# Performance work log

Measured on AMD Instinct MI355X. Metric: run time of the kernel, lower is better.

The kernel has to match this reference:

```python
import jax, jax.numpy as jnp
import numpy as np

B, D = 16384, 512
NUM_CLASSES, K = 90, 32


def _l2norm(v, axis=-1):
    return v / jnp.sqrt(jnp.sum(v * v, axis=axis, keepdims=True) + 1e-12)


def setup_inputs() -> dict:
    key = jax.random.key(0)
    k1, k2, k3 = jax.random.split(key, 3)
    x = jax.random.normal(k1, (B, D), dtype=jnp.float32)
    labels = jax.random.randint(k2, (B,), 0, NUM_CLASSES, dtype=jnp.int64)
    centers = jax.random.normal(k3, (NUM_CLASSES, K, D), dtype=jnp.float32)
    return {"x": x, "labels": labels, "centers": centers}


def reference(x, labels, centers):
    # l2Norm applied to centers at init and to x in forward
    xn = _l2norm(x, axis=1)                       # [B, D]
    cn = _l2norm(centers, axis=-1)                # [C, K, D]
    c = cn[labels]                                # gather: [B, K, D]
    # dst_k = 1 - <x_b, center_{label_b, k}>
    dst = 1.0 - jnp.einsum("bd,bkd->bk", xn, c)   # [B, K]
    score = jax.nn.softmax(2.0 - dst, axis=1)     # softmax over K sub-centers
    per_sample = jnp.sum(score * dst, axis=1)     # [B]
    return jnp.mean(per_sample)                   # scalar loss
```

## Files before the change

### kernel.cpp

```cpp
#include <hip/hip_runtime.h>
#include <hip/hip_bf16.h>

#define BB 16384
#define DD 512
#define NCLS 90
#define KC 32
#define BUCKET 512
#define PRB 180

typedef __attribute__((ext_vector_type(8))) short short8;
typedef __attribute__((ext_vector_type(4))) float fx4;

static __device__ __forceinline__ short f2bf(float f) {
    unsigned u = __float_as_uint(f);
    unsigned r = (u + 0x7fffu + ((u >> 16) & 1u)) >> 16;
    return (short)r;
}
static __device__ __forceinline__ short8 pack8(float4 a, float4 b) {
    union { __hip_bfloat162 h[4]; short8 s; } u;
    u.h[0] = __float22bfloat162_rn(make_float2(a.x, a.y));
    u.h[1] = __float22bfloat162_rn(make_float2(a.z, a.w));
    u.h[2] = __float22bfloat162_rn(make_float2(b.x, b.y));
    u.h[3] = __float22bfloat162_rn(make_float2(b.z, b.w));
    return u.s;
}
static __device__ __forceinline__ void gload_lds16(const void* g, void* l) {
    __builtin_amdgcn_global_load_lds(
        (const __attribute__((address_space(1))) void*)g,
        (__attribute__((address_space(3))) void*)l, 16, 0, 0);
}

__global__ __launch_bounds__(1024)
void k_prep(const float* __restrict__ centers, const int* __restrict__ labels,
            short* __restrict__ cni, int* __restrict__ idx, int* __restrict__ cnt) {
    __shared__ int lab[BB];
    __shared__ int wcnt[16];

    int t = threadIdx.x, w = t >> 6, lane = t & 63;

    if ((int)blockIdx.x < PRB) {
        int row = blockIdx.x * 16 + w;
        const float4* p = (const float4*)(centers + (size_t)row * DD);
        float4 a = p[lane * 2];
        float4 b = p[lane * 2 + 1];
        float s = a.x * a.x + a.y * a.y + a.z * a.z + a.w * a.w
                + b.x * b.x + b.y * b.y + b.z * b.z + b.w * b.w;
#pragma unroll
        for (int m = 1; m < 64; m <<= 1) s += __shfl_xor(s, m, 64);
        float sc = rsqrtf(s + 1e-12f);
        short8 v;
        v[0] = f2bf(a.x * sc); v[1] = f2bf(a.y * sc);
        v[2] = f2bf(a.z * sc); v[3] = f2bf(a.w * sc);
        v[4] = f2bf(b.x * sc); v[5] = f2bf(b.y * sc);
        v[6] = f2bf(b.z * sc); v[7] = f2bf(b.w * sc);
        *(short8*)(cni + (size_t)row * DD + lane * 8) = v;
    } else {
        int c = blockIdx.x - PRB;
        for (int j = t; j < BB / 4; j += 1024)
            ((int4*)lab)[j] = ((const int4*)labels)[j];
        __syncthreads();

        int seg4 = w * (BB / 4 / 16);
        int cw = 0;
#pragma unroll
        for (int jj = 0; jj < 4; jj++) {
            int4 v = ((int4*)lab)[seg4 + jj * 64 + lane];
            cw += (v.x == c) + (v.y == c) + (v.z == c) + (v.w == c);
        }
#pragma unroll
        for (int m = 1; m < 64; m <<= 1) cw += __shfl_xor(cw, m, 64);
        if (lane == 0) wcnt[w] = cw;
        __syncthreads();
        int pos = c * BUCKET;
        for (int ww = 0; ww < w; ww++) pos += wcnt[ww];
#pragma unroll
        for (int jj = 0; jj < 4; jj++) {
            int4 v = ((int4*)lab)[seg4 + jj * 64 + lane];
            int gbase = (seg4 + jj * 64 + lane) * 4;
            { bool m = (v.x == c); unsigned long long k = __ballot(m);
              if (m) idx[pos + __popcll(k & ((1ull << lane) - 1ull))] = gbase;     pos += __popcll(k); }
            { bool m = (v.y == c); unsigned long long k = __ballot(m);
              if (m) idx[pos + __popcll(k & ((1ull << lane) - 1ull))] = gbase + 1; pos += __popcll(k); }
            { bool m = (v.z == c); unsigned long long k = __ballot(m);
              if (m) idx[pos + __popcll(k & ((1ull << lane) - 1ull))] = gbase + 2; pos += __popcll(k); }
            { bool m = (v.w == c); unsigned long long k = __ballot(m);
              if (m) idx[pos + __popcll(k & ((1ull << lane) - 1ull))] = gbase + 3; pos += __popcll(k); }
        }
        if (t == 0) {
            int s = 0;
#pragma unroll
            for (int i = 0; i < 16; i++) s += wcnt[i];
            cnt[c] = s;
        }
    }
}

__launch_bounds__(256, 2)
__global__ void k_main(const float* __restrict__ x,
                       const short* __restrict__ cni,
                       const int* __restrict__ cnt,
                       const int* __restrict__ idx,
                       float* __restrict__ partials) {
    __shared__ __align__(16) short c_lds[KC * DD];
    __shared__ __align__(16) short x_lds[32 * DD];
    __shared__ float S_lds[32][33];
    __shared__ float xinv[32];
    __shared__ float red[256];

    int c = blockIdx.x >> 3;
    int p = blockIdx.x & 7;
    int n = cnt[c];
    int nch = (n + 31) >> 5;
    int t = threadIdx.x, w = t >> 6, lane = t & 63;
    float loss_acc = 0.f;

    if (p < nch) {
        const short* cbase = cni + (size_t)c * KC * DD;
#pragma unroll
        for (int it = 0; it < 8; it++) {
            int q = t + 256 * it;
            int drow = q >> 6, cc = q & 63;
            gload_lds16(cbase + drow * DD + (cc ^ (drow & 7)) * 8, &c_lds[q * 8]);
        }

        int base = c * BUCKET;
        int mrow = ((w & 1) << 4) + (lane & 15);
        int nrow = ((w >> 1) << 4) + (lane & 15);
        int row8 = t >> 3, l8 = t & 7;

        for (int ch = p; ch < nch; ch += 8) {
            int off = ch << 5;
            int rem = n - off;

            {
                int r = (row8 < rem) ? row8 : (rem - 1);
                int g = idx[base + off + r];
                const float4* src = (const float4*)(x + (size_t)g * DD);
                float4 va[8], vb[8];
#pragma unroll
                for (int jj = 0; jj < 8; jj++) {
                    va[jj] = src[2 * l8 + 16 * jj];
                    vb[jj] = src[2 * l8 + 16 * jj + 1];
                }
                float nrm = 0.f;
#pragma unroll
                for (int jj = 0; jj < 8; jj++) {
                    int cc = l8 + 8 * jj;
                    float4 a = va[jj], b = vb[jj];
                    nrm += a.x * a.x + a.y * a.y + a.z * a.z + a.w * a.w
                         + b.x * b.x + b.y * b.y + b.z * b.z + b.w * b.w;
                    *(short8*)&x_lds[row8 * DD + ((cc ^ (row8 & 7)) << 3)] = pack8(a, b);
                }
#pragma unroll
                for (int m = 1; m < 8; m <<= 1) nrm += __shfl_xor(nrm, m, 64);
                if (l8 == 0) xinv[row8] = rsqrtf(nrm + 1e-12f);
            }
            __syncthreads();

            fx4 acc = {0.f, 0.f, 0.f, 0.f};
#pragma unroll
            for (int ks = 0; ks < 16; ks++) {
                int c16a = ks * 4 + (lane >> 4);
                short8 av = *(const short8*)&x_lds[mrow * DD + ((c16a ^ (mrow & 7)) << 3)];
                short8 bv = *(const short8*)&c_lds[nrow * DD + ((c16a ^ (nrow & 7)) << 3)];
                acc = __builtin_amdgcn_mfma_f32_16x16x32_bf16(av, bv, acc, 0, 0, 0);
            }
#pragma unroll
            for (int j = 0; j < 4; j++) {
                int r = ((w & 1) << 4) + ((lane >> 4) << 2) + j;
                int col = ((w >> 1) << 4) + (lane & 15);
                S_lds[r][col] = acc[j];
            }
            __syncthreads();

            {
                float xv = xinv[row8];
                int q4 = l8 << 2;
                float s0 = S_lds[row8][q4 + 0] * xv;
                float s1 = S_lds[row8][q4 + 1] * xv;
                float s2 = S_lds[row8][q4 + 2] * xv;
                float s3 = S_lds[row8][q4 + 3] * xv;
                float mx = fmaxf(fmaxf(s0, s1), fmaxf(s2, s3));
#pragma unroll
                for (int m = 1; m < 8; m <<= 1) mx = fmaxf(mx, __shfl_xor(mx, m, 64));
                float e0 = expf(s0 - mx), e1 = expf(s1 - mx);
                float e2 = expf(s2 - mx), e3 = expf(s3 - mx);
                float Z = e0 + e1 + e2 + e3;
                float num = e0 * (1.f - s0) + e1 * (1.f - s1)
                          + e2 * (1.f - s2) + e3 * (1.f - s3);
#pragma unroll
                for (int m = 1; m < 8; m <<= 1) {
                    Z += __shfl_xor(Z, m, 64);
                    num += __shfl_xor(num, m, 64);
                }
                if (l8 == 0 && row8 < rem) loss_acc += num / Z;
            }
            __syncthreads();
        }
    }

    red[t] = loss_acc;
    __syncthreads();
    for (int h = 128; h > 0; h >>= 1) {
        if (t < h) red[t] += red[t + h];
        __syncthreads();
    }
    if (t == 0) partials[blockIdx.x] = red[0];
}

__global__ void k_final(const float* __restrict__ partials, float* __restrict__ out) {
    __shared__ float red[256];
    int t = threadIdx.x;
    float s = 0.f;
    for (int i = t; i < NCLS * 8; i += 256) s += partials[i];
    red[t] = s;
    __syncthreads();
    for (int h = 128; h > 0; h >>= 1) {
        if (t < h) red[t] += red[t + h];
        __syncthreads();
    }
    if (t == 0) out[0] = red[0] * (1.0f / (float)BB);
}

extern "C" void kernel_launch(void* const* d_in, const int* in_sizes, int n_in,
                              void* d_out, int out_size, void* d_ws, size_t ws_size,
                              hipStream_t stream) {
    const float* x       = (const float*)d_in[0];
    const int*   labels  = (const int*)d_in[1];
    const float* centers = (const float*)d_in[2];
    float* out = (float*)d_out;

    char* ws = (char*)d_ws;
    short* cni      = (short*)(ws + 0);
    int*   idx      = (int*)(ws + 3145728);
    int*   cnt      = (int*)(ws + 3407872);
    float* partials = (float*)(ws + 3473408);

    k_prep<<<PRB + NCLS, 1024, 0, stream>>>(centers, labels, cni, idx, cnt);
    k_main<<<NCLS * 8, 256, 0, stream>>>(x, cni, cnt, idx, partials);
    k_final<<<1, 256, 0, stream>>>(partials, out);
}
```

Measured before the change: 27.86 us.

## Scatter x into class-sorted bf16 buffer in separate streaming kernel

Replaces the gather of fp32 x rows inside the main kernel with a new streaming kernel. It reads x in row order, normalises each row, converts it to bf16 and scatters it into a per-class bucketed, swizzled layout together with the inverse norms. The main kernel then fills LDS with contiguous async global-to-LDS loads instead of indexed fp32 loads plus conversion. This costs one extra kernel launch and an extra bf16 write and read of x (about 16 MB through global memory), but makes the main kernel's loads coalesced and halves their size.

```diff
diff --git a/kernel.cpp b/kernel.cpp
--- a/kernel.cpp
+++ b/kernel.cpp
@@ -32,7 +32,7 @@
 
 __global__ __launch_bounds__(1024)
 void k_prep(const float* __restrict__ centers, const int* __restrict__ labels,
-            short* __restrict__ cni, int* __restrict__ idx, int* __restrict__ cnt) {
+            short* __restrict__ cni, int* __restrict__ dest, int* __restrict__ cnt) {
     __shared__ int lab[BB];
     __shared__ int wcnt[16];
 
@@ -78,13 +78,13 @@
             int4 v = ((int4*)lab)[seg4 + jj * 64 + lane];
             int gbase = (seg4 + jj * 64 + lane) * 4;
             { bool m = (v.x == c); unsigned long long k = __ballot(m);
-              if (m) idx[pos + __popcll(k & ((1ull << lane) - 1ull))] = gbase;     pos += __popcll(k); }
+              if (m) dest[gbase]     = pos + __popcll(k & ((1ull << lane) - 1ull)); pos += __popcll(k); }
             { bool m = (v.y == c); unsigned long long k = __ballot(m);
-              if (m) idx[pos + __popcll(k & ((1ull << lane) - 1ull))] = gbase + 1; pos += __popcll(k); }
+              if (m) dest[gbase + 1] = pos + __popcll(k & ((1ull << lane) - 1ull)); pos += __popcll(k); }
             { bool m = (v.z == c); unsigned long long k = __ballot(m);
-              if (m) idx[pos + __popcll(k & ((1ull << lane) - 1ull))] = gbase + 2; pos += __popcll(k); }
+              if (m) dest[gbase + 2] = pos + __popcll(k & ((1ull << lane) - 1ull)); pos += __popcll(k); }
             { bool m = (v.w == c); unsigned long long k = __ballot(m);
-              if (m) idx[pos + __popcll(k & ((1ull << lane) - 1ull))] = gbase + 3; pos += __popcll(k); }
+              if (m) dest[gbase + 3] = pos + __popcll(k & ((1ull << lane) - 1ull)); pos += __popcll(k); }
         }
         if (t == 0) {
             int s = 0;
@@ -95,16 +95,32 @@
     }
 }
 
+__global__ __launch_bounds__(1024)
+void k_stream(const float* __restrict__ x, const int* __restrict__ dest,
+              short* __restrict__ xb, float* __restrict__ xinv) {
+    int row = blockIdx.x * 16 + (threadIdx.x >> 6);
+    int lane = threadIdx.x & 63;
+    int slot = dest[row];
+    const float4* p = (const float4*)(x + (size_t)row * DD);
+    float4 a = p[lane * 2];
+    float4 b = p[lane * 2 + 1];
+    float s = a.x * a.x + a.y * a.y + a.z * a.z + a.w * a.w
+            + b.x * b.x + b.y * b.y + b.z * b.z + b.w * b.w;
+#pragma unroll
+    for (int m = 1; m < 64; m <<= 1) s += __shfl_xor(s, m, 64);
+    *(short8*)(xb + (size_t)slot * DD + ((lane ^ (slot & 7)) << 3)) = pack8(a, b);
+    if (lane == 0) xinv[slot] = rsqrtf(s + 1e-12f);
+}
+
 __launch_bounds__(256, 2)
-__global__ void k_main(const float* __restrict__ x,
+__global__ void k_main(const short* __restrict__ xb,
+                       const float* __restrict__ xinv_g,
                        const short* __restrict__ cni,
                        const int* __restrict__ cnt,
-                       const int* __restrict__ idx,
                        float* __restrict__ partials) {
     __shared__ __align__(16) short c_lds[KC * DD];
     __shared__ __align__(16) short x_lds[32 * DD];
     __shared__ float S_lds[32][33];
-    __shared__ float xinv[32];
     __shared__ float red[256];
 
     int c = blockIdx.x >> 3;
@@ -123,7 +139,6 @@
             gload_lds16(cbase + drow * DD + (cc ^ (drow & 7)) * 8, &c_lds[q * 8]);
         }
 
-        int base = c * BUCKET;
         int mrow = ((w & 1) << 4) + (lane & 15);
         int nrow = ((w >> 1) << 4) + (lane & 15);
         int row8 = t >> 3, l8 = t & 7;
@@ -132,29 +147,13 @@
             int off = ch << 5;
             int rem = n - off;
 
-            {
-                int r = (row8 < rem) ? row8 : (rem - 1);
-                int g = idx[base + off + r];
-                const float4* src = (const float4*)(x + (size_t)g * DD);
-                float4 va[8], vb[8];
-#pragma unroll
-                for (int jj = 0; jj < 8; jj++) {
-                    va[jj] = src[2 * l8 + 16 * jj];
-                    vb[jj] = src[2 * l8 + 16 * jj + 1];
-                }
-                float nrm = 0.f;
-#pragma unroll
-                for (int jj = 0; jj < 8; jj++) {
-                    int cc = l8 + 8 * jj;
-                    float4 a = va[jj], b = vb[jj];
-                    nrm += a.x * a.x + a.y * a.y + a.z * a.z + a.w * a.w
-                         + b.x * b.x + b.y * b.y + b.z * b.z + b.w * b.w;
-                    *(short8*)&x_lds[row8 * DD + ((cc ^ (row8 & 7)) << 3)] = pack8(a, b);
-                }
-#pragma unroll
-                for (int m = 1; m < 8; m <<= 1) nrm += __shfl_xor(nrm, m, 64);
-                if (l8 == 0) xinv[row8] = rsqrtf(nrm + 1e-12f);
-            }
+            const short* xbase = xb + (size_t)(c * BUCKET + off) * DD;
+#pragma unroll
+            for (int it = 0; it < 8; it++) {
+                int q = t + 256 * it;
+                gload_lds16(xbase + q * 8, &x_lds[q * 8]);
+            }
+            float xv = xinv_g[c * BUCKET + off + row8];
             __syncthreads();
 
             fx4 acc = {0.f, 0.f, 0.f, 0.f};
@@ -174,7 +173,6 @@
             __syncthreads();
 
             {
-                float xv = xinv[row8];
                 int q4 = l8 << 2;
                 float s0 = S_lds[row8][q4 + 0] * xv;
                 float s1 = S_lds[row8][q4 + 1] * xv;
@@ -232,11 +230,14 @@
 
     char* ws = (char*)d_ws;
     short* cni      = (short*)(ws + 0);
-    int*   idx      = (int*)(ws + 3145728);
-    int*   cnt      = (int*)(ws + 3407872);
-    float* partials = (float*)(ws + 3473408);
-
-    k_prep<<<PRB + NCLS, 1024, 0, stream>>>(centers, labels, cni, idx, cnt);
-    k_main<<<NCLS * 8, 256, 0, stream>>>(x, cni, cnt, idx, partials);
+    short* xb       = (short*)(ws + (4u << 20));
+    float* xinv     = (float*)(ws + (56u << 20));
+    int*   dest     = (int*)(ws + (57u << 20));
+    int*   cnt      = (int*)(ws + (58u << 20));
+    float* partials = (float*)(ws + (58u << 20) + 4096);
+
+    k_prep<<<PRB + NCLS, 1024, 0, stream>>>(centers, labels, cni, dest, cnt);
+    k_stream<<<BB / 16, 1024, 0, stream>>>(x, dest, xb, xinv);
+    k_main<<<NCLS * 8, 256, 0, stream>>>(xb, xinv, cni, cnt, partials);
     k_final<<<1, 256, 0, stream>>>(partials, out);
 }
```

Result: slower. 34.31 us (+23.2%).
